# Performance work log

Hardware: AMD Instinct MI355X
Metric: run time of the kernel (lower is better)

## Reference

```python
import jax, jax.numpy as jnp
import numpy as np
import math

B, N, D, H, O = 2, 1024, 256, 4, 8
DT, STEPS = 0.1, 5


def setup_inputs() -> dict:
    key = jax.random.key(0)
    ks = jax.random.split(key, 8)
    inv_d = 1.0 / math.sqrt(D)
    inv_ho = 1.0 / math.sqrt(H * O)
    return {
        "x": jax.random.normal(ks[0], (B, N, D), jnp.float32),
        "Wq": jax.random.normal(ks[1], (D, D), jnp.float32) * inv_d,
        "Wk": jax.random.normal(ks[2], (D, D), jnp.float32) * inv_d,
        "Wp": jax.random.normal(ks[3], (H * O, D), jnp.float32) * inv_d,
        "bp": jnp.zeros((H * O,), jnp.float32),
        "Wo": jax.random.normal(ks[4], (D, H * O), jnp.float32) * inv_ho,
        "bo": jnp.zeros((D,), jnp.float32),
        "omega": jax.random.normal(ks[5], (H, O), jnp.float32) * 0.1,
        "coupling_scale": jnp.asarray(1.0, jnp.float32),
    }


def reference(x, Wq, Wk, Wp, bp, Wo, bo, omega, coupling_scale):
    dk = D // H
    # attention coupling J_ij = softmax(q_i.k_j / sqrt(d_k))  -> (B,H,N,N)
    q = (x @ Wq.T).reshape(B, N, H, dk).transpose(0, 2, 1, 3)
    k = (x @ Wk.T).reshape(B, N, H, dk).transpose(0, 2, 1, 3)
    J = jax.nn.softmax(jnp.einsum('bhid,bhjd->bhij', q, k) / math.sqrt(dk), axis=-1)
    # initial phases (B,H,N,O)
    phases = (x @ Wp.T + bp).reshape(B, N, H, O).transpose(0, 2, 1, 3)
    om = omega[None, :, None, :]  # (1,H,1,O)

    def step(ph, _):
        # sum_j J_ij sin(phi_j - phi_i) = cos(phi_i)*(J@sin phi) - sin(phi_i)*(J@cos phi)
        s, c = jnp.sin(ph), jnp.cos(ph)
        coupling = c * jnp.einsum('bhij,bhjo->bhio', J, s) - s * jnp.einsum('bhij,bhjo->bhio', J, c)
        new = ph + DT * (om + coupling_scale * coupling)
        new = jnp.remainder(new + jnp.pi, 2 * jnp.pi) - jnp.pi
        return new, None

    phases, _ = jax.lax.scan(step, phases, None, length=STEPS)
    sig = jnp.cos(phases).transpose(0, 2, 1, 3).reshape(B, N, H * O)
    return sig @ Wo.T + bo
```

## Files before the change

kernel.cpp:

```cpp
#include <hip/hip_runtime.h>
#include <hip/hip_bf16.h>
#include <math.h>


#define NB 1024
#define NH 4
#define DD 256
#define NO 8
#define PI_F      3.14159265358979323846f
#define TWO_PI_F  6.28318530717958647692f
#define INV_2PI_F 0.15915494309189533577f

typedef __attribute__((ext_vector_type(8))) short bf16x8;
typedef __attribute__((ext_vector_type(4))) float f32x4;

__device__ __forceinline__ float b2f_u(unsigned short s) {
    union { unsigned u; float f; } x; x.u = ((unsigned)s) << 16; return x.f;
}
__device__ __forceinline__ unsigned short f2b(float f) {
    union { float f; unsigned u; } v; v.f = f;
    unsigned r = v.u + 0x7FFFu + ((v.u >> 16) & 1u);
    return (unsigned short)(r >> 16);
}
template<bool F32>
__device__ __forceinline__ uint4 load_pack8(const void* p, size_t off) {
    if (!F32) return *(const uint4*)((const unsigned short*)p + off);
    const float* fp = (const float*)p + off;
    float4 a = *(const float4*)fp;
    float4 b = *(const float4*)(fp + 4);
    uint4 r;
    r.x = (unsigned)f2b(a.x) | ((unsigned)f2b(a.y) << 16);
    r.y = (unsigned)f2b(a.z) | ((unsigned)f2b(a.w) << 16);
    r.z = (unsigned)f2b(b.x) | ((unsigned)f2b(b.y) << 16);
    r.w = (unsigned)f2b(b.z) | ((unsigned)f2b(b.w) << 16);
    return r;
}
__device__ __forceinline__ void load8_rt(int f32, const void* p, int i, float* f) {
    if (f32) {
        const float* fp = (const float*)p + i;
        float4 a = *(const float4*)fp;
        float4 b = *(const float4*)(fp + 4);
        f[0]=a.x; f[1]=a.y; f[2]=a.z; f[3]=a.w;
        f[4]=b.x; f[5]=b.y; f[6]=b.z; f[7]=b.w;
    } else {
        uint4 u = *(const uint4*)((const unsigned short*)p + i);
        f[0] = b2f_u(u.x & 0xFFFFu); f[1] = b2f_u(u.x >> 16);
        f[2] = b2f_u(u.y & 0xFFFFu); f[3] = b2f_u(u.y >> 16);
        f[4] = b2f_u(u.z & 0xFFFFu); f[5] = b2f_u(u.z >> 16);
        f[6] = b2f_u(u.w & 0xFFFFu); f[7] = b2f_u(u.w >> 16);
    }
}
__device__ __forceinline__ float read_cs_bf16(const void* p) {
    float vb = b2f_u(*(const unsigned short*)p);
    bool ok = isfinite(vb) && fabsf(vb) > 1e-30f && fabsf(vb) < 1e30f;
    if (ok) return vb;
    return *(const float*)p;
}
__device__ __forceinline__ int detect_inline(const unsigned short* x) {
    int l = threadIdx.x & 63;
    float a0 = fabsf(b2f_u(x[2 * l]));
    float a1 = fabsf(b2f_u(x[2 * (l + 64)]));
    unsigned long long b0 = __ballot(!(a0 >= 1e-10f && a0 <= 100.0f));
    unsigned long long b1 = __ballot(!(a1 >= 1e-10f && a1 <= 100.0f));
    return (__popcll(b0) + __popcll(b1)) > 16;
}

template<bool F32>
__device__ void projm_impl(
    const void* __restrict__ x, const void* __restrict__ Wq,
    const void* __restrict__ Wk, const void* __restrict__ Wp,
    const void* __restrict__ bp,
    unsigned short* __restrict__ Qb, unsigned short* __restrict__ Kb,
    float* __restrict__ PH, unsigned short* __restrict__ SC)
{
    __shared__ uint4 Xsh[64 * 32];
    __shared__ uint4 Wsh[64 * 32];
    const int tid = threadIdx.x;
    const int ftile = blockIdx.x % 9, itile = blockIdx.x / 9;
    const int i0 = itile * 64, f0 = ftile * 64;
    const int wave = tid >> 6, lane = tid & 63;
    const int n = lane & 15, quad = lane >> 4;

    #pragma unroll
    for (int g = 0; g < 8; g++) {
        int fidx = g * 256 + tid;
        int row = fidx >> 5, q = fidx & 31;
        int sw = (q & 24) | ((q ^ row) & 7);
        Xsh[row * 32 + sw] = load_pack8<F32>(x, (size_t)(i0 + row) * 256 + q * 8);
        int wr = f0 + row;
        uint4 wv = make_uint4(0, 0, 0, 0);
        if (wr < 256)      wv = load_pack8<F32>(Wq, (size_t)wr * 256 + q * 8);
        else if (wr < 512) wv = load_pack8<F32>(Wk, (size_t)(wr - 256) * 256 + q * 8);
        else if (wr < 544) wv = load_pack8<F32>(Wp, (size_t)(wr - 512) * 256 + q * 8);
        Wsh[row * 32 + sw] = wv;
    }
    __syncthreads();

    f32x4 acc[4];
    #pragma unroll
    for (int s = 0; s < 4; s++) acc[s] = (f32x4){0.f, 0.f, 0.f, 0.f};
    const int xrow = wave * 16 + n;
    #pragma unroll
    for (int s = 0; s < 8; s++) {
        int qc = s * 4 + quad;
        bf16x8 b = ((const bf16x8*)Xsh)[xrow * 32 + ((qc & 24) | ((qc ^ xrow) & 7))];
        #pragma unroll
        for (int sub = 0; sub < 4; sub++) {
            int wr = sub * 16 + n;
            bf16x8 a = ((const bf16x8*)Wsh)[wr * 32 + ((qc & 24) | ((qc ^ wr) & 7))];
            acc[sub] = __builtin_amdgcn_mfma_f32_16x16x32_bf16(a, b, acc[sub], 0, 0, 0);
        }
    }

    const int ig = i0 + wave * 16 + n;
    const int bb = ig >> 10, nr = ig & 1023;
    if (ftile < 4) {
        #pragma unroll
        for (int sub = 0; sub < 4; sub++) {
            int dd = sub * 16 + quad * 4;
            ushort4 v = make_ushort4(f2b(acc[sub][0] * 0.125f), f2b(acc[sub][1] * 0.125f),
                                     f2b(acc[sub][2] * 0.125f), f2b(acc[sub][3] * 0.125f));
            *(ushort4*)(Qb + ((size_t)((bb * NH + ftile) * NB + nr)) * 64 + dd) = v;
        }
    } else if (ftile < 8) {
        int h = ftile - 4;
        #pragma unroll
        for (int sub = 0; sub < 4; sub++) {
            int dd = sub * 16 + quad * 4;
            ushort4 v = make_ushort4(f2b(acc[sub][0]), f2b(acc[sub][1]),
                                     f2b(acc[sub][2]), f2b(acc[sub][3]));
            *(ushort4*)(Kb + ((size_t)((bb * NH + h) * NB + nr)) * 64 + dd) = v;
        }
    } else {
        #pragma unroll
        for (int sub = 0; sub < 2; sub++) {
            #pragma unroll
            for (int r = 0; r < 4; r++) {
                int fp = sub * 16 + quad * 4 + r;
                int h2 = fp >> 3, o = fp & 7;
                float bpv = F32 ? ((const float*)bp)[fp]
                                : b2f_u(((const unsigned short*)bp)[fp]);
                float v = acc[sub][r] + bpv;
                int bh = bb * NH + h2;
                PH[(size_t)bh * 8192 + o * 1024 + nr] = v;
                float sv, cv;
                __sincosf(v, &sv, &cv);
                SC[(size_t)(bh * 16 + o) * 1024 + nr]     = f2b(sv);
                SC[(size_t)(bh * 16 + 8 + o) * 1024 + nr] = f2b(cv);
            }
        }
    }
}

__global__ __launch_bounds__(256) void k_projm(
    const unsigned short* x, const void* Wq, const void* Wk, const void* Wp,
    const void* bp, unsigned short* Qb, unsigned short* Kb, float* PH,
    unsigned short* SC)
{
    if (detect_inline(x)) projm_impl<true >(x, Wq, Wk, Wp, bp, Qb, Kb, PH, SC);
    else                  projm_impl<false>(x, Wq, Wk, Wp, bp, Qb, Kb, PH, SC);
}

__global__ __launch_bounds__(256) void k_scores(
    const unsigned short* __restrict__ Qb, const unsigned short* __restrict__ Kb,
    unsigned short* __restrict__ U, float* __restrict__ R)
{
    __shared__ float redS[4][16];
    const int tid = threadIdx.x;
    const int bh  = blockIdx.x >> 6;
    const int i0  = (blockIdx.x & 63) * 16;
    const int wave = tid >> 6, lane = tid & 63;
    const int n = lane & 15, quad = lane >> 4;

    const unsigned short* qrow = Qb + ((size_t)(bh * NB) + i0 + n) * 64;
    bf16x8 bq0 = *(const bf16x8*)(qrow + quad * 8);
    bf16x8 bq1 = *(const bf16x8*)(qrow + 32 + quad * 8);

    float s = 0.f;
    unsigned short* urow = U + ((size_t)(bh * NB) + i0 + n) * NB;
    const unsigned short* kbase = Kb + ((size_t)(bh * NB) + n) * 64;
    #pragma unroll 2
    for (int t = 0; t < 16; t++) {
        int jt = wave * 16 + t;
        const unsigned short* arow = kbase + (size_t)jt * 16 * 64;
        bf16x8 a0 = *(const bf16x8*)(arow + quad * 8);
        bf16x8 a1 = *(const bf16x8*)(arow + 32 + quad * 8);
        f32x4 acc = {0.f, 0.f, 0.f, 0.f};
        acc = __builtin_amdgcn_mfma_f32_16x16x32_bf16(a0, bq0, acc, 0, 0, 0);
        acc = __builtin_amdgcn_mfma_f32_16x16x32_bf16(a1, bq1, acc, 0, 0, 0);
        float u0 = __expf(acc[0]);
        float u1 = __expf(acc[1]);
        float u2 = __expf(acc[2]);
        float u3 = __expf(acc[3]);
        s += (u0 + u1) + (u2 + u3);
        *(ushort4*)(urow + jt * 16 + quad * 4)
            = make_ushort4(f2b(u0), f2b(u1), f2b(u2), f2b(u3));
    }
    s += __shfl_xor(s, 16);
    s += __shfl_xor(s, 32);
    if (lane < 16) redS[wave][lane] = s;
    __syncthreads();
    if (wave == 0 && lane < 16)
        R[bh * NB + i0 + lane]
            = 1.0f / (redS[0][lane] + redS[1][lane] + redS[2][lane] + redS[3][lane]);
}

__global__ __launch_bounds__(256) void k_step(
    const unsigned short* __restrict__ xraw,
    const unsigned short* __restrict__ U, const float* __restrict__ R,
    const float* __restrict__ PHin, float* __restrict__ PHout,
    const unsigned short* __restrict__ SCin, unsigned short* __restrict__ SCout,
    const void* __restrict__ omega, const void* __restrict__ csp)
{
    __shared__ f32x4 red[4][64];
    const int tid  = threadIdx.x;
    const int bh   = blockIdx.x >> 6;
    const int i0   = (blockIdx.x & 63) * 16;
    const int wave = tid >> 6, lane = tid & 63;
    const int n    = lane & 15, quad = lane >> 4;
    const int f32  = detect_inline(xraw);
    const float* phs = PHin + (size_t)bh * 8192;

    const unsigned short* urow  = U + ((size_t)(bh * NB) + i0 + n) * NB;
    const unsigned short* scrow = SCin + (size_t)(bh * 16 + n) * 1024;
    f32x4 acc = {0.f, 0.f, 0.f, 0.f};
    #pragma unroll
    for (int t = 0; t < 8; t++) {
        int it = wave * 8 + t;
        bf16x8 a = *(const bf16x8*)(urow  + it * 32 + quad * 8);
        bf16x8 b = *(const bf16x8*)(scrow + it * 32 + quad * 8);
        acc = __builtin_amdgcn_mfma_f32_16x16x32_bf16(a, b, acc, 0, 0, 0);
    }
    red[wave][lane] = acc;
    __syncthreads();

    if (wave == 0) {
        f32x4 a0 = red[0][lane], a1 = red[1][lane];
        f32x4 a2 = red[2][lane], a3 = red[3][lane];
        #pragma unroll
        for (int v = 0; v < 4; v++) acc[v] = (a0[v] + a1[v]) + (a2[v] + a3[v]);

        float C0 = __shfl_xor(acc[0], 8);
        float C1 = __shfl_xor(acc[1], 8);
        float C2 = __shfl_xor(acc[2], 8);
        float C3 = __shfl_xor(acc[3], 8);

        if (n < 8) {
            const int o = n, h = bh & 3;
            const float cs = f32 ? *(const float*)csp : read_cs_bf16(csp);
            const float om = f32 ? ((const float*)omega)[h * NO + o]
                                 : b2f_u(((const unsigned short*)omega)[h * NO + o]);
            float4 Rv = *(const float4*)(R + bh * NB + i0 + quad * 4);
            float4 pv = *(const float4*)(phs + o * 1024 + i0 + quad * 4);
            float S[4] = {acc[0], acc[1], acc[2], acc[3]};
            float C[4] = {C0, C1, C2, C3};
            float Rr[4] = {Rv.x, Rv.y, Rv.z, Rv.w};
            float P[4]  = {pv.x, pv.y, pv.z, pv.w};
            float op[4];
            #pragma unroll
            for (int r = 0; r < 4; r++) {
                float si, ci;
                __sincosf(P[r], &si, &ci);
                float coup = (ci * S[r] - si * C[r]) * Rr[r];
                float v = P[r] + 0.1f * (om + cs * coup);
                float t2 = v + PI_F;
                t2 -= floorf(t2 * INV_2PI_F) * TWO_PI_F;
                op[r] = t2 - PI_F;
            }
            *(float4*)(PHout + (size_t)bh * 8192 + o * 1024 + i0 + quad * 4)
                = make_float4(op[0], op[1], op[2], op[3]);
            #pragma unroll
            for (int r = 0; r < 4; r++) {
                float sn, cn;
                __sincosf(op[r], &sn, &cn);
                int i = i0 + quad * 4 + r;
                SCout[(size_t)(bh * 16 + o) * 1024 + i]     = f2b(sn);
                SCout[(size_t)(bh * 16 + 8 + o) * 1024 + i] = f2b(cn);
            }
        }
    }
}

__global__ __launch_bounds__(256) void k_out(
    const unsigned short* __restrict__ xraw,
    const unsigned short* __restrict__ SC,
    const void* __restrict__ Wo, const void* __restrict__ bo,
    void* __restrict__ out)
{
    __shared__ float sig[32];
    const int tid = threadIdx.x;
    const int b = blockIdx.x >> 10, n = blockIdx.x & 1023;
    const int f32 = detect_inline(xraw);
    if (tid < 32) {
        int h = tid >> 3, o = tid & 7;
        sig[tid] = b2f_u(SC[(size_t)((b * NH + h) * 16 + 8 + o) * 1024 + n]);
    }
    __syncthreads();
    float acc = f32 ? ((const float*)bo)[tid] : b2f_u(((const unsigned short*)bo)[tid]);
    #pragma unroll
    for (int d0 = 0; d0 < 32; d0 += 8) {
        float w[8];
        load8_rt(f32, Wo, tid * 32 + d0, w);
        #pragma unroll
        for (int t = 0; t < 8; t++) acc += sig[d0 + t] * w[t];
    }
    size_t oi = (size_t)blockIdx.x * DD + tid;
    if (f32) ((float*)out)[oi] = acc;
    else     ((unsigned short*)out)[oi] = f2b(acc);
}

extern "C" void kernel_launch(void* const* d_in, const int* in_sizes, int n_in,
                              void* d_out, int out_size, void* d_ws, size_t ws_size,
                              hipStream_t stream)
{
    const unsigned short* x = (const unsigned short*)d_in[0];
    const void* Wq  = d_in[1];
    const void* Wk  = d_in[2];
    const void* Wp  = d_in[3];
    const void* bp  = d_in[4];
    const void* Wo  = d_in[5];
    const void* bo  = d_in[6];
    const void* om  = d_in[7];
    const void* cs  = d_in[8];

    char* w = (char*)d_ws;
    unsigned short* Qb  = (unsigned short*)w;
    unsigned short* Kb  = (unsigned short*)(w + (1u << 20));
    float*          R   = (float*)(w + (2u << 20));
    float*          PH0 = (float*)(w + (2u << 20) + (64u << 10));
    float*          PH1 = (float*)(w + (2u << 20) + (320u << 10));
    unsigned short* SC0 = (unsigned short*)(w + (2u << 20) + (576u << 10));
    unsigned short* SC1 = (unsigned short*)(w + (2u << 20) + (832u << 10));
    unsigned short* U   = (unsigned short*)(w + (2u << 20) + (1088u << 10));

    k_projm <<<288, 256, 0, stream>>>(x, Wq, Wk, Wp, bp, Qb, Kb, PH0, SC0);
    k_scores<<<512, 256, 0, stream>>>(Qb, Kb, U, R);
    k_step<<<512, 256, 0, stream>>>(x, U, R, PH0, PH1, SC0, SC1, om, cs);
    k_step<<<512, 256, 0, stream>>>(x, U, R, PH1, PH0, SC1, SC0, om, cs);
    k_step<<<512, 256, 0, stream>>>(x, U, R, PH0, PH1, SC0, SC1, om, cs);
    k_step<<<512, 256, 0, stream>>>(x, U, R, PH1, PH0, SC1, SC0, om, cs);
    k_step<<<512, 256, 0, stream>>>(x, U, R, PH0, PH1, SC0, SC1, om, cs);
    k_out<<<2048, 256, 0, stream>>>(x, SC1, Wo, bo, d_out);
}
```

Before: 142.6 us.

## Fuse score computation with first Kuramoto step and batch output rows per block

The score kernel now also runs the first phase-update step: it keeps its 16 rows of unnormalized attention weights in swizzled shared memory and multiplies them with the sin/cos table directly, so one kernel launch and one full read of U from global memory go away. The output projection now handles 8 rows per block with Wo held in registers, cutting the block count and Wo reloads. The cost is more shared memory and registers in the fused kernel, which may lower occupancy.

```diff
diff --git a/kernel.cpp b/kernel.cpp
--- a/kernel.cpp
+++ b/kernel.cpp
@@ -161,25 +161,33 @@
     else                  projm_impl<false>(x, Wq, Wk, Wp, bp, Qb, Kb, PH, SC);
 }
 
-__global__ __launch_bounds__(256) void k_scores(
+__global__ __launch_bounds__(256) void k_scores_step1(
+    const unsigned short* __restrict__ xraw,
     const unsigned short* __restrict__ Qb, const unsigned short* __restrict__ Kb,
-    unsigned short* __restrict__ U, float* __restrict__ R)
-{
+    unsigned short* __restrict__ U, float* __restrict__ R,
+    const float* __restrict__ PHin, float* __restrict__ PHout,
+    const unsigned short* __restrict__ SCin, unsigned short* __restrict__ SCout,
+    const void* __restrict__ omega, const void* __restrict__ csp)
+{
+    __shared__ uint4 Ush[16 * 128];
+    __shared__ f32x4 red[4][64];
     __shared__ float redS[4][16];
+    __shared__ float Rsh[16];
     const int tid = threadIdx.x;
     const int bh  = blockIdx.x >> 6;
     const int i0  = (blockIdx.x & 63) * 16;
     const int wave = tid >> 6, lane = tid & 63;
     const int n = lane & 15, quad = lane >> 4;
+    const int f32 = detect_inline(xraw);
+    const float* phs = PHin + (size_t)bh * 8192;
 
     const unsigned short* qrow = Qb + ((size_t)(bh * NB) + i0 + n) * 64;
     bf16x8 bq0 = *(const bf16x8*)(qrow + quad * 8);
     bf16x8 bq1 = *(const bf16x8*)(qrow + 32 + quad * 8);
-
     float s = 0.f;
     unsigned short* urow = U + ((size_t)(bh * NB) + i0 + n) * NB;
     const unsigned short* kbase = Kb + ((size_t)(bh * NB) + n) * 64;
-    #pragma unroll 2
+    #pragma unroll
     for (int t = 0; t < 16; t++) {
         int jt = wave * 16 + t;
         const unsigned short* arow = kbase + (size_t)jt * 16 * 64;
@@ -193,16 +201,78 @@
         float u2 = __expf(acc[2]);
         float u3 = __expf(acc[3]);
         s += (u0 + u1) + (u2 + u3);
-        *(ushort4*)(urow + jt * 16 + quad * 4)
-            = make_ushort4(f2b(u0), f2b(u1), f2b(u2), f2b(u3));
+        ushort4 uv = make_ushort4(f2b(u0), f2b(u1), f2b(u2), f2b(u3));
+        *(ushort4*)(urow + jt * 16 + quad * 4) = uv;
+        int cw = 2 * jt + (quad >> 1);
+        ((ushort4*)Ush)[(n * 128 + (cw ^ (n & 7))) * 2 + (quad & 1)] = uv;
     }
     s += __shfl_xor(s, 16);
     s += __shfl_xor(s, 32);
     if (lane < 16) redS[wave][lane] = s;
     __syncthreads();
-    if (wave == 0 && lane < 16)
-        R[bh * NB + i0 + lane]
-            = 1.0f / (redS[0][lane] + redS[1][lane] + redS[2][lane] + redS[3][lane]);
+    if (tid < 16) {
+        float rv = 1.0f / (redS[0][tid] + redS[1][tid] + redS[2][tid] + redS[3][tid]);
+        Rsh[tid] = rv;
+        R[bh * NB + i0 + tid] = rv;
+    }
+
+    const unsigned short* scrow = SCin + (size_t)(bh * 16 + n) * 1024;
+    f32x4 acc = {0.f, 0.f, 0.f, 0.f};
+    #pragma unroll
+    for (int t = 0; t < 8; t++) {
+        int it = wave * 8 + t;
+        bf16x8 a = ((const bf16x8*)Ush)[n * 128 + ((it * 4 + quad) ^ (n & 7))];
+        bf16x8 b = *(const bf16x8*)(scrow + it * 32 + quad * 8);
+        acc = __builtin_amdgcn_mfma_f32_16x16x32_bf16(a, b, acc, 0, 0, 0);
+    }
+    red[wave][lane] = acc;
+    __syncthreads();
+
+    if (wave == 0) {
+        f32x4 a0 = red[0][lane], a1 = red[1][lane];
+        f32x4 a2 = red[2][lane], a3 = red[3][lane];
+        #pragma unroll
+        for (int v = 0; v < 4; v++) acc[v] = (a0[v] + a1[v]) + (a2[v] + a3[v]);
+
+        float C0 = __shfl_xor(acc[0], 8);
+        float C1 = __shfl_xor(acc[1], 8);
+        float C2 = __shfl_xor(acc[2], 8);
+        float C3 = __shfl_xor(acc[3], 8);
+
+        if (n < 8) {
+            const int o = n, h = bh & 3;
+            const float cs = f32 ? *(const float*)csp : read_cs_bf16(csp);
+            const float om = f32 ? ((const float*)omega)[h * NO + o]
+                                 : b2f_u(((const unsigned short*)omega)[h * NO + o]);
+            float4 pv = *(const float4*)(phs + o * 1024 + i0 + quad * 4);
+            float S[4] = {acc[0], acc[1], acc[2], acc[3]};
+            float C[4] = {C0, C1, C2, C3};
+            float Rr[4] = {Rsh[quad * 4], Rsh[quad * 4 + 1],
+                           Rsh[quad * 4 + 2], Rsh[quad * 4 + 3]};
+            float P[4]  = {pv.x, pv.y, pv.z, pv.w};
+            float op[4];
+            #pragma unroll
+            for (int r = 0; r < 4; r++) {
+                float si, ci;
+                __sincosf(P[r], &si, &ci);
+                float coup = (ci * S[r] - si * C[r]) * Rr[r];
+                float v = P[r] + 0.1f * (om + cs * coup);
+                float t2 = v + PI_F;
+                t2 -= floorf(t2 * INV_2PI_F) * TWO_PI_F;
+                op[r] = t2 - PI_F;
+            }
+            *(float4*)(PHout + (size_t)bh * 8192 + o * 1024 + i0 + quad * 4)
+                = make_float4(op[0], op[1], op[2], op[3]);
+            #pragma unroll
+            for (int r = 0; r < 4; r++) {
+                float sn, cn;
+                __sincosf(op[r], &sn, &cn);
+                int i = i0 + quad * 4 + r;
+                SCout[(size_t)(bh * 16 + o) * 1024 + i]     = f2b(sn);
+                SCout[(size_t)(bh * 16 + 8 + o) * 1024 + i] = f2b(cn);
+            }
+        }
+    }
 }
 
 __global__ __launch_bounds__(256) void k_step(
@@ -287,26 +357,33 @@
     const void* __restrict__ Wo, const void* __restrict__ bo,
     void* __restrict__ out)
 {
-    __shared__ float sig[32];
+    __shared__ float sig[8 * 32];
     const int tid = threadIdx.x;
-    const int b = blockIdx.x >> 10, n = blockIdx.x & 1023;
+    const int b  = blockIdx.x >> 7;
+    const int n0 = (blockIdx.x & 127) * 8;
     const int f32 = detect_inline(xraw);
-    if (tid < 32) {
-        int h = tid >> 3, o = tid & 7;
-        sig[tid] = b2f_u(SC[(size_t)((b * NH + h) * 16 + 8 + o) * 1024 + n]);
+
+    {
+        int r = tid >> 5, f = tid & 31;
+        int h = f >> 3, o = f & 7;
+        sig[r * 32 + f] = b2f_u(SC[(size_t)((b * NH + h) * 16 + 8 + o) * 1024 + n0 + r]);
     }
     __syncthreads();
-    float acc = f32 ? ((const float*)bo)[tid] : b2f_u(((const unsigned short*)bo)[tid]);
-    #pragma unroll
-    for (int d0 = 0; d0 < 32; d0 += 8) {
-        float w[8];
-        load8_rt(f32, Wo, tid * 32 + d0, w);
-        #pragma unroll
-        for (int t = 0; t < 8; t++) acc += sig[d0 + t] * w[t];
-    }
-    size_t oi = (size_t)blockIdx.x * DD + tid;
-    if (f32) ((float*)out)[oi] = acc;
-    else     ((unsigned short*)out)[oi] = f2b(acc);
+
+    float wv[32];
+    #pragma unroll
+    for (int d0 = 0; d0 < 32; d0 += 8) load8_rt(f32, Wo, tid * 32 + d0, wv + d0);
+    const float bov = f32 ? ((const float*)bo)[tid] : b2f_u(((const unsigned short*)bo)[tid]);
+
+    #pragma unroll
+    for (int r = 0; r < 8; r++) {
+        float acc = bov;
+        #pragma unroll
+        for (int t = 0; t < 32; t++) acc += sig[r * 32 + t] * wv[t];
+        size_t oi = ((size_t)b * 1024 + n0 + r) * DD + tid;
+        if (f32) ((float*)out)[oi] = acc;
+        else     ((unsigned short*)out)[oi] = f2b(acc);
+    }
 }
 
 extern "C" void kernel_launch(void* const* d_in, const int* in_sizes, int n_in,
@@ -333,12 +410,11 @@
     unsigned short* SC1 = (unsigned short*)(w + (2u << 20) + (832u << 10));
     unsigned short* U   = (unsigned short*)(w + (2u << 20) + (1088u << 10));
 
-    k_projm <<<288, 256, 0, stream>>>(x, Wq, Wk, Wp, bp, Qb, Kb, PH0, SC0);
-    k_scores<<<512, 256, 0, stream>>>(Qb, Kb, U, R);
-    k_step<<<512, 256, 0, stream>>>(x, U, R, PH0, PH1, SC0, SC1, om, cs);
+    k_projm<<<288, 256, 0, stream>>>(x, Wq, Wk, Wp, bp, Qb, Kb, PH0, SC0);
+    k_scores_step1<<<512, 256, 0, stream>>>(x, Qb, Kb, U, R, PH0, PH1, SC0, SC1, om, cs);
     k_step<<<512, 256, 0, stream>>>(x, U, R, PH1, PH0, SC1, SC0, om, cs);
     k_step<<<512, 256, 0, stream>>>(x, U, R, PH0, PH1, SC0, SC1, om, cs);
     k_step<<<512, 256, 0, stream>>>(x, U, R, PH1, PH0, SC1, SC0, om, cs);
     k_step<<<512, 256, 0, stream>>>(x, U, R, PH0, PH1, SC0, SC1, om, cs);
-    k_out<<<2048, 256, 0, stream>>>(x, SC1, Wo, bo, d_out);
-}
+    k_out<<<256, 256, 0, stream>>>(x, SC1, Wo, bo, d_out);
+}
```

After: 134.7 us. 1.06x faster.

## Fuse scores, all ODE steps and output projection into one persistent kernel

Applied to the files above, without the earlier changes.

Merges the scores kernel, the five step kernels and the output kernel into a single 512-block kernel. Each block keeps its softmax numerator rows in LDS with an XOR swizzle instead of writing the NxN matrix to global memory. Blocks synchronise between steps with a global atomic-counter barrier, and phases stay in registers. This removes six launches and the repeated global reads of U, but the barrier relies on all 512 blocks being resident at once and has a spin timeout that could silently break correctness.

```diff
diff --git a/kernel.cpp b/kernel.cpp
--- a/kernel.cpp
+++ b/kernel.cpp
@@ -155,31 +155,42 @@
 __global__ __launch_bounds__(256) void k_projm(
     const unsigned short* x, const void* Wq, const void* Wk, const void* Wp,
     const void* bp, unsigned short* Qb, unsigned short* Kb, float* PH,
-    unsigned short* SC)
+    unsigned short* SC, unsigned int* ctr)
 {
+    if (blockIdx.x == 0 && threadIdx.x < 8) ctr[threadIdx.x] = 0u;
     if (detect_inline(x)) projm_impl<true >(x, Wq, Wk, Wp, bp, Qb, Kb, PH, SC);
     else                  projm_impl<false>(x, Wq, Wk, Wp, bp, Qb, Kb, PH, SC);
 }
 
-__global__ __launch_bounds__(256) void k_scores(
+__global__ __launch_bounds__(256) void k_mega2(
+    const unsigned short* __restrict__ xraw,
     const unsigned short* __restrict__ Qb, const unsigned short* __restrict__ Kb,
-    unsigned short* __restrict__ U, float* __restrict__ R)
+    const float* __restrict__ PH0,
+    unsigned short* __restrict__ SC0, unsigned short* __restrict__ SCA,
+    const void* __restrict__ omega, const void* __restrict__ csp,
+    const void* __restrict__ Wo, const void* __restrict__ bo,
+    void* __restrict__ out, unsigned int* __restrict__ ctr)
 {
+    __shared__ uint4 Ush[16 * 128];
+    __shared__ f32x4 red[4][64];
     __shared__ float redS[4][16];
+    __shared__ float Rsh[16];
+    __shared__ float sig[4][32];
+
     const int tid = threadIdx.x;
-    const int bh  = blockIdx.x >> 6;
-    const int i0  = (blockIdx.x & 63) * 16;
+    const int bid = blockIdx.x;
+    const int bh  = bid >> 6;
+    const int i0  = (bid & 63) * 16;
     const int wave = tid >> 6, lane = tid & 63;
     const int n = lane & 15, quad = lane >> 4;
+    const int f32 = detect_inline(xraw);
 
     const unsigned short* qrow = Qb + ((size_t)(bh * NB) + i0 + n) * 64;
     bf16x8 bq0 = *(const bf16x8*)(qrow + quad * 8);
     bf16x8 bq1 = *(const bf16x8*)(qrow + 32 + quad * 8);
-
     float s = 0.f;
-    unsigned short* urow = U + ((size_t)(bh * NB) + i0 + n) * NB;
     const unsigned short* kbase = Kb + ((size_t)(bh * NB) + n) * 64;
-    #pragma unroll 2
+    #pragma unroll
     for (int t = 0; t < 16; t++) {
         int jt = wave * 16 + t;
         const unsigned short* arow = kbase + (size_t)jt * 16 * 64;
@@ -193,120 +204,113 @@
         float u2 = __expf(acc[2]);
         float u3 = __expf(acc[3]);
         s += (u0 + u1) + (u2 + u3);
-        *(ushort4*)(urow + jt * 16 + quad * 4)
-            = make_ushort4(f2b(u0), f2b(u1), f2b(u2), f2b(u3));
+        ushort4 uv = make_ushort4(f2b(u0), f2b(u1), f2b(u2), f2b(u3));
+        int cw = 2 * jt + (quad >> 1);
+        ((ushort4*)Ush)[(n * 128 + (cw ^ (n & 7))) * 2 + (quad & 1)] = uv;
     }
     s += __shfl_xor(s, 16);
     s += __shfl_xor(s, 32);
     if (lane < 16) redS[wave][lane] = s;
     __syncthreads();
-    if (wave == 0 && lane < 16)
-        R[bh * NB + i0 + lane]
-            = 1.0f / (redS[0][lane] + redS[1][lane] + redS[2][lane] + redS[3][lane]);
-}
-
-__global__ __launch_bounds__(256) void k_step(
-    const unsigned short* __restrict__ xraw,
-    const unsigned short* __restrict__ U, const float* __restrict__ R,
-    const float* __restrict__ PHin, float* __restrict__ PHout,
-    const unsigned short* __restrict__ SCin, unsigned short* __restrict__ SCout,
-    const void* __restrict__ omega, const void* __restrict__ csp)
-{
-    __shared__ f32x4 red[4][64];
-    const int tid  = threadIdx.x;
-    const int bh   = blockIdx.x >> 6;
-    const int i0   = (blockIdx.x & 63) * 16;
-    const int wave = tid >> 6, lane = tid & 63;
-    const int n    = lane & 15, quad = lane >> 4;
-    const int f32  = detect_inline(xraw);
-    const float* phs = PHin + (size_t)bh * 8192;
-
-    const unsigned short* urow  = U + ((size_t)(bh * NB) + i0 + n) * NB;
-    const unsigned short* scrow = SCin + (size_t)(bh * 16 + n) * 1024;
-    f32x4 acc = {0.f, 0.f, 0.f, 0.f};
-    #pragma unroll
-    for (int t = 0; t < 8; t++) {
-        int it = wave * 8 + t;
-        bf16x8 a = *(const bf16x8*)(urow  + it * 32 + quad * 8);
-        bf16x8 b = *(const bf16x8*)(scrow + it * 32 + quad * 8);
-        acc = __builtin_amdgcn_mfma_f32_16x16x32_bf16(a, b, acc, 0, 0, 0);
-    }
-    red[wave][lane] = acc;
+    if (tid < 16)
+        Rsh[tid] = 1.0f / (redS[0][tid] + redS[1][tid] + redS[2][tid] + redS[3][tid]);
+
+    float P[4];
+    float cs_ = 0.f, om_ = 0.f;
+    if (wave == 0 && n < 8) {
+        const int o = n, h = bh & 3;
+        cs_ = f32 ? *(const float*)csp : read_cs_bf16(csp);
+        om_ = f32 ? ((const float*)omega)[h * NO + o]
+                  : b2f_u(((const unsigned short*)omega)[h * NO + o]);
+        float4 pv = *(const float4*)(PH0 + (size_t)bh * 8192 + o * 1024 + i0 + quad * 4);
+        P[0] = pv.x; P[1] = pv.y; P[2] = pv.z; P[3] = pv.w;
+    }
+
+    unsigned short* scin  = SC0;
+    unsigned short* scout = SCA;
+
+    #pragma unroll 1
+    for (int k = 0; k < 5; k++) {
+        const unsigned short* scrow = scin + (size_t)(bh * 16 + n) * 1024;
+        f32x4 acc = {0.f, 0.f, 0.f, 0.f};
+        #pragma unroll
+        for (int t = 0; t < 8; t++) {
+            int it = wave * 8 + t;
+            bf16x8 a = ((const bf16x8*)Ush)[n * 128 + ((it * 4 + quad) ^ (n & 7))];
+            bf16x8 b = *(const bf16x8*)(scrow + it * 32 + quad * 8);
+            acc = __builtin_amdgcn_mfma_f32_16x16x32_bf16(a, b, acc, 0, 0, 0);
+        }
+        red[wave][lane] = acc;
+        __syncthreads();
+
+        if (wave == 0) {
+            f32x4 a0 = red[0][lane], a1 = red[1][lane];
+            f32x4 a2 = red[2][lane], a3 = red[3][lane];
+            #pragma unroll
+            for (int v = 0; v < 4; v++) acc[v] = (a0[v] + a1[v]) + (a2[v] + a3[v]);
+            float C0 = __shfl_xor(acc[0], 8);
+            float C1 = __shfl_xor(acc[1], 8);
+            float C2 = __shfl_xor(acc[2], 8);
+            float C3 = __shfl_xor(acc[3], 8);
+            if (n < 8) {
+                const int o = n;
+                float S[4] = {acc[0], acc[1], acc[2], acc[3]};
+                float C[4] = {C0, C1, C2, C3};
+                float Rr[4] = {Rsh[quad * 4], Rsh[quad * 4 + 1],
+                               Rsh[quad * 4 + 2], Rsh[quad * 4 + 3]};
+                #pragma unroll
+                for (int r = 0; r < 4; r++) {
+                    float si, ci;
+                    __sincosf(P[r], &si, &ci);
+                    float coup = (ci * S[r] - si * C[r]) * Rr[r];
+                    float v = P[r] + 0.1f * (om_ + cs_ * coup);
+                    float t2 = v + PI_F;
+                    t2 -= floorf(t2 * INV_2PI_F) * TWO_PI_F;
+                    P[r] = t2 - PI_F;
+                    float sn, cn;
+                    __sincosf(P[r], &sn, &cn);
+                    int i = i0 + quad * 4 + r;
+                    scout[(size_t)(bh * 16 + o) * 1024 + i]     = f2b(sn);
+                    scout[(size_t)(bh * 16 + 8 + o) * 1024 + i] = f2b(cn);
+                }
+            }
+        }
+        __syncthreads();
+        if (tid == 0) {
+            __threadfence();
+            atomicAdd(&ctr[k], 1u);
+            unsigned spins = 0;
+            while (__hip_atomic_load(&ctr[k], __ATOMIC_RELAXED,
+                                     __HIP_MEMORY_SCOPE_AGENT) < 512u) {
+                __builtin_amdgcn_s_sleep(8);
+                if (++spins > (1u << 20)) break;
+            }
+        }
+        __syncthreads();
+        __threadfence();
+        unsigned short* tmp = scin; scin = scout; scout = tmp;
+    }
+
+    const int ob = bid >> 8, n0 = (bid & 255) * 4;
+    if (tid < 128) {
+        int r = tid >> 5, f = tid & 31;
+        int h = f >> 3, o = f & 7;
+        sig[r][f] = b2f_u(scin[(size_t)((ob * NH + h) * 16 + 8 + o) * 1024 + n0 + r]);
+    }
     __syncthreads();
-
-    if (wave == 0) {
-        f32x4 a0 = red[0][lane], a1 = red[1][lane];
-        f32x4 a2 = red[2][lane], a3 = red[3][lane];
-        #pragma unroll
-        for (int v = 0; v < 4; v++) acc[v] = (a0[v] + a1[v]) + (a2[v] + a3[v]);
-
-        float C0 = __shfl_xor(acc[0], 8);
-        float C1 = __shfl_xor(acc[1], 8);
-        float C2 = __shfl_xor(acc[2], 8);
-        float C3 = __shfl_xor(acc[3], 8);
-
-        if (n < 8) {
-            const int o = n, h = bh & 3;
-            const float cs = f32 ? *(const float*)csp : read_cs_bf16(csp);
-            const float om = f32 ? ((const float*)omega)[h * NO + o]
-                                 : b2f_u(((const unsigned short*)omega)[h * NO + o]);
-            float4 Rv = *(const float4*)(R + bh * NB + i0 + quad * 4);
-            float4 pv = *(const float4*)(phs + o * 1024 + i0 + quad * 4);
-            float S[4] = {acc[0], acc[1], acc[2], acc[3]};
-            float C[4] = {C0, C1, C2, C3};
-            float Rr[4] = {Rv.x, Rv.y, Rv.z, Rv.w};
-            float P[4]  = {pv.x, pv.y, pv.z, pv.w};
-            float op[4];
-            #pragma unroll
-            for (int r = 0; r < 4; r++) {
-                float si, ci;
-                __sincosf(P[r], &si, &ci);
-                float coup = (ci * S[r] - si * C[r]) * Rr[r];
-                float v = P[r] + 0.1f * (om + cs * coup);
-                float t2 = v + PI_F;
-                t2 -= floorf(t2 * INV_2PI_F) * TWO_PI_F;
-                op[r] = t2 - PI_F;
-            }
-            *(float4*)(PHout + (size_t)bh * 8192 + o * 1024 + i0 + quad * 4)
-                = make_float4(op[0], op[1], op[2], op[3]);
-            #pragma unroll
-            for (int r = 0; r < 4; r++) {
-                float sn, cn;
-                __sincosf(op[r], &sn, &cn);
-                int i = i0 + quad * 4 + r;
-                SCout[(size_t)(bh * 16 + o) * 1024 + i]     = f2b(sn);
-                SCout[(size_t)(bh * 16 + 8 + o) * 1024 + i] = f2b(cn);
-            }
-        }
-    }
-}
-
-__global__ __launch_bounds__(256) void k_out(
-    const unsigned short* __restrict__ xraw,
-    const unsigned short* __restrict__ SC,
-    const void* __restrict__ Wo, const void* __restrict__ bo,
-    void* __restrict__ out)
-{
-    __shared__ float sig[32];
-    const int tid = threadIdx.x;
-    const int b = blockIdx.x >> 10, n = blockIdx.x & 1023;
-    const int f32 = detect_inline(xraw);
-    if (tid < 32) {
-        int h = tid >> 3, o = tid & 7;
-        sig[tid] = b2f_u(SC[(size_t)((b * NH + h) * 16 + 8 + o) * 1024 + n]);
-    }
-    __syncthreads();
-    float acc = f32 ? ((const float*)bo)[tid] : b2f_u(((const unsigned short*)bo)[tid]);
-    #pragma unroll
-    for (int d0 = 0; d0 < 32; d0 += 8) {
-        float w[8];
-        load8_rt(f32, Wo, tid * 32 + d0, w);
-        #pragma unroll
-        for (int t = 0; t < 8; t++) acc += sig[d0 + t] * w[t];
-    }
-    size_t oi = (size_t)blockIdx.x * DD + tid;
-    if (f32) ((float*)out)[oi] = acc;
-    else     ((unsigned short*)out)[oi] = f2b(acc);
+    float wv[32];
+    #pragma unroll
+    for (int d0 = 0; d0 < 32; d0 += 8) load8_rt(f32, Wo, tid * 32 + d0, wv + d0);
+    const float bov = f32 ? ((const float*)bo)[tid] : b2f_u(((const unsigned short*)bo)[tid]);
+    #pragma unroll
+    for (int r = 0; r < 4; r++) {
+        float acc = bov;
+        #pragma unroll
+        for (int t = 0; t < 32; t++) acc += sig[r][t] * wv[t];
+        size_t oi = ((size_t)ob * 1024 + n0 + r) * DD + tid;
+        if (f32) ((float*)out)[oi] = acc;
+        else     ((unsigned short*)out)[oi] = f2b(acc);
+    }
 }
 
 extern "C" void kernel_launch(void* const* d_in, const int* in_sizes, int n_in,
@@ -326,19 +330,12 @@
     char* w = (char*)d_ws;
     unsigned short* Qb  = (unsigned short*)w;
     unsigned short* Kb  = (unsigned short*)(w + (1u << 20));
-    float*          R   = (float*)(w + (2u << 20));
-    float*          PH0 = (float*)(w + (2u << 20) + (64u << 10));
-    float*          PH1 = (float*)(w + (2u << 20) + (320u << 10));
-    unsigned short* SC0 = (unsigned short*)(w + (2u << 20) + (576u << 10));
-    unsigned short* SC1 = (unsigned short*)(w + (2u << 20) + (832u << 10));
-    unsigned short* U   = (unsigned short*)(w + (2u << 20) + (1088u << 10));
-
-    k_projm <<<288, 256, 0, stream>>>(x, Wq, Wk, Wp, bp, Qb, Kb, PH0, SC0);
-    k_scores<<<512, 256, 0, stream>>>(Qb, Kb, U, R);
-    k_step<<<512, 256, 0, stream>>>(x, U, R, PH0, PH1, SC0, SC1, om, cs);
-    k_step<<<512, 256, 0, stream>>>(x, U, R, PH1, PH0, SC1, SC0, om, cs);
-    k_step<<<512, 256, 0, stream>>>(x, U, R, PH0, PH1, SC0, SC1, om, cs);
-    k_step<<<512, 256, 0, stream>>>(x, U, R, PH1, PH0, SC1, SC0, om, cs);
-    k_step<<<512, 256, 0, stream>>>(x, U, R, PH0, PH1, SC0, SC1, om, cs);
-    k_out<<<2048, 256, 0, stream>>>(x, SC1, Wo, bo, d_out);
-}
+    float*          PH0 = (float*)(w + (2u << 20));
+    unsigned short* SC0 = (unsigned short*)(w + (2u << 20) + (256u << 10));
+    unsigned short* SCA = (unsigned short*)(w + (2u << 20) + (512u << 10));
+    unsigned int*   ctr = (unsigned int*)(w + (3u << 20));
+
+    k_projm<<<288, 256, 0, stream>>>(x, Wq, Wk, Wp, bp, Qb, Kb, PH0, SC0, ctr);
+    k_mega2<<<512, 256, 0, stream>>>(x, Qb, Kb, PH0, SC0, SCA, om, cs,
+                                     Wo, bo, d_out, ctr);
+}
```

After: 436.6 us. 206% more time.
